# Performance work log

Measured on AMD Instinct MI355X. Metric: run time of the kernel, lower is better.

Reference implementation:

```python
import jax, jax.numpy as jnp
import numpy as np

NUM_HEADS = 32
KV_HEADS = 8
HEAD_SIZE = 128
BATCH = 32
BLOCK_SIZE = 16
BLOCKS_PER_SEQ = 128
NUM_BLOCKS = BATCH * BLOCKS_PER_SEQ  # 4096
ROPE_BASE = 10000.0


def _rope(x, pos):
    # x: [B, n_heads, D]; pos: [B] int32 -> rotate per-sequence single token
    d = x.shape[-1]
    inv_freq = 1.0 / (ROPE_BASE ** (jnp.arange(0, d, 2, dtype=jnp.float32) / d))  # [D/2]
    freqs = pos.astype(jnp.float32)[:, None] * inv_freq[None, :]                  # [B, D/2]
    emb = jnp.concatenate([freqs, freqs], axis=-1)                                # [B, D]
    cos = jnp.cos(emb)[:, None, :]
    sin = jnp.sin(emb)[:, None, :]
    x1, x2 = x[..., : d // 2], x[..., d // 2 :]
    rotated = jnp.concatenate([-x2, x1], axis=-1)
    return x * cos + rotated * sin


def setup_inputs() -> dict:
    key = jax.random.key(0)
    ks = jax.random.split(key, 6)
    query = jax.random.normal(ks[0], (BATCH, NUM_HEADS, HEAD_SIZE), dtype=jnp.float32)
    k_new = jax.random.normal(ks[1], (BATCH, KV_HEADS, HEAD_SIZE), dtype=jnp.float32)
    v_new = jax.random.normal(ks[2], (BATCH, KV_HEADS, HEAD_SIZE), dtype=jnp.float32)
    k_cache = jax.random.normal(ks[3], (NUM_BLOCKS, BLOCK_SIZE, KV_HEADS, HEAD_SIZE), dtype=jnp.float32)
    v_cache = jax.random.normal(ks[4], (NUM_BLOCKS, BLOCK_SIZE, KV_HEADS, HEAD_SIZE), dtype=jnp.float32)
    # each sequence owns a contiguous run of blocks
    block_tables = jnp.arange(NUM_BLOCKS, dtype=jnp.int32).reshape(BATCH, BLOCKS_PER_SEQ)
    context_lens = jax.random.randint(ks[5], (BATCH,), 0, 2047, dtype=jnp.int32)
    return {
        "query": query,
        "key": k_new,
        "value": v_new,
        "k_cache": k_cache,
        "v_cache": v_cache,
        "block_tables": block_tables,
        "context_lens": context_lens,
    }


def reference(query, key, value, k_cache, v_cache, block_tables, context_lens):
    B, H, D = query.shape
    KVH = key.shape[1]
    G = H // KVH
    scale = 1.0 / (D ** 0.5)

    # --- RoPE: source uses position = context_len + 1 for both q and k ---
    pos = context_lens + 1
    q = _rope(query, pos)   # [B, H, D]
    k = _rope(key, pos)     # [B, KVH, D]

    # --- scatter new token into the paged KV cache at slot = context_len ---
    slot = context_lens                               # [B]
    blk = jnp.take_along_axis(block_tables, (slot // BLOCK_SIZE)[:, None], axis=1)[:, 0]
    off = slot % BLOCK_SIZE
    k_cache = k_cache.at[blk, off].set(k)
    v_cache = v_cache.at[blk, off].set(value)

    # --- gather this batch's pages: [B, T, KVH, D] with T = blocks*block_size ---
    T = BLOCKS_PER_SEQ * BLOCK_SIZE
    K = k_cache[block_tables].reshape(B, T, KVH, D)
    V = v_cache[block_tables].reshape(B, T, KVH, D)

    # --- GQA single-query attention over cache_seqlens = context_len + 1 ---
    qg = q.reshape(B, KVH, G, D)
    scores = jnp.einsum("bhgd,bthd->bhgt", qg, K) * scale            # [B, KVH, G, T]
    valid = (jnp.arange(T, dtype=jnp.int32)[None, :] < (context_lens + 1)[:, None])
    scores = jnp.where(valid[:, None, None, :], scores, -jnp.inf)
    probs = jax.nn.softmax(scores, axis=-1)
    out = jnp.einsum("bhgt,bthd->bhgd", probs, V)                    # [B, KVH, G, D]
    return out.reshape(B, H, D)
```

## Files before the change

### kernel.cpp

```cpp
#include <hip/hip_runtime.h>
#include <math.h>

#define BATCH    32
#define NHEADS   32
#define KVHEADS  8
#define GRP      4
#define HSZ      128
#define BLKSZ    16
#define BPS      128
#define NTHREADS 512
#define NPROC    16
#define CHUNK    256
#define NSPLIT   8
#define SCALE    0.08838834764831843f

__device__ __forceinline__ void proc_row(const float4 kv, const float4 vv,
                                         const float4* qf, float* m, float* l,
                                         float4* o) {
    float s[GRP];
#pragma unroll
    for (int g = 0; g < GRP; ++g)
        s[g] = qf[g].x * kv.x + qf[g].y * kv.y + qf[g].z * kv.z + qf[g].w * kv.w;
#pragma unroll
    for (int g = 0; g < GRP; ++g) {
        s[g] += __shfl_xor(s[g], 1);
        s[g] += __shfl_xor(s[g], 2);
        s[g] += __shfl_xor(s[g], 4);
        s[g] += __shfl_xor(s[g], 8);
        s[g] += __shfl_xor(s[g], 16);
    }
#pragma unroll
    for (int g = 0; g < GRP; ++g) {
        const float sc = s[g] * SCALE;
        const float mn = fmaxf(m[g], sc);
        const float cf = __expf(m[g] - mn);
        const float pp = __expf(sc - mn);
        l[g] = l[g] * cf + pp;
        o[g].x = o[g].x * cf + pp * vv.x;
        o[g].y = o[g].y * cf + pp * vv.y;
        o[g].z = o[g].z * cf + pp * vv.z;
        o[g].w = o[g].w * cf + pp * vv.w;
        m[g] = mn;
    }
}

__global__ __launch_bounds__(NTHREADS) void pa_partial(
    const float* __restrict__ query,
    const float* __restrict__ k_new,
    const float* __restrict__ v_new,
    const float* __restrict__ k_cache,
    const float* __restrict__ v_cache,
    const int*  __restrict__ block_tables,
    const int*  __restrict__ ctx_lens,
    float* __restrict__ pm, float* __restrict__ pl, float* __restrict__ po)
{
    const int wg    = blockIdx.x;
    const int chunk = wg & (NSPLIT - 1);
    const int kvh   = (wg >> 3) & (KVHEADS - 1);
    const int b     = wg >> 6;
    const int ctx   = ctx_lens[b];
    const int t0    = chunk * CHUNK;
    if (t0 > ctx) return;

    const int tid  = threadIdx.x;
    const int sub  = tid & 31;
    const int proc = tid >> 5;

    __shared__ float q_s[GRP][HSZ];
    __shared__ float kn_s[HSZ];
    __shared__ int   bt_s[CHUNK / BLKSZ];
    __shared__ float m_s[NPROC][GRP];
    __shared__ float l_s[NPROC][GRP];
    __shared__ float o_s[NPROC][GRP][HSZ];

    {
        const float p = (float)(ctx + 1);
        if (tid < 320) {
            const int   i    = tid & 63;
            const float invf = exp2f(-((float)i / 64.0f) * 13.287712379549449f);
            float s_, c_;
            sincosf(p * invf, &s_, &c_);
            if (tid < 256) {
                const int g = tid >> 6;
                const float* qp = query + ((size_t)b * NHEADS + kvh * GRP + g) * HSZ;
                const float x1 = qp[i], x2 = qp[i + 64];
                q_s[g][i]      = x1 * c_ - x2 * s_;
                q_s[g][i + 64] = x2 * c_ + x1 * s_;
            } else {
                const float* kp = k_new + ((size_t)b * KVHEADS + kvh) * HSZ;
                const float x1 = kp[i], x2 = kp[i + 64];
                kn_s[i]      = x1 * c_ - x2 * s_;
                kn_s[i + 64] = x2 * c_ + x1 * s_;
            }
        } else if (tid < 320 + CHUNK / BLKSZ) {
            bt_s[tid - 320] = block_tables[b * BPS + (t0 >> 4) + (tid - 320)];
        }
    }
    __syncthreads();

    const int d0 = sub << 2;
    float4 qf[GRP];
#pragma unroll
    for (int g = 0; g < GRP; ++g) qf[g] = *(const float4*)&q_s[g][d0];

    float  m[GRP], l[GRP];
    float4 o[GRP];
#pragma unroll
    for (int g = 0; g < GRP; ++g) {
        m[g] = -INFINITY; l[g] = 0.f;
        o[g] = make_float4(0.f, 0.f, 0.f, 0.f);
    }

    const int tend = min(t0 + CHUNK, ctx);
    int t = t0 + proc;
    for (; t + NPROC < tend; t += 2 * NPROC) {
        const int    blk0 = bt_s[(t - t0) >> 4];
        const int    blk1 = bt_s[((t - t0) >> 4) + 1];
        const int    off  = t & 15;
        const size_t a0 = (((size_t)blk0 * BLKSZ + off) * KVHEADS + kvh) * HSZ + d0;
        const size_t a1 = (((size_t)blk1 * BLKSZ + off) * KVHEADS + kvh) * HSZ + d0;
        const float4 kv0 = *(const float4*)(k_cache + a0);
        const float4 vv0 = *(const float4*)(v_cache + a0);
        const float4 kv1 = *(const float4*)(k_cache + a1);
        const float4 vv1 = *(const float4*)(v_cache + a1);
        proc_row(kv0, vv0, qf, m, l, o);
        proc_row(kv1, vv1, qf, m, l, o);
    }
    for (; t < tend; t += NPROC) {
        const int    blk  = bt_s[(t - t0) >> 4];
        const size_t a0 = (((size_t)blk * BLKSZ + (t & 15)) * KVHEADS + kvh) * HSZ + d0;
        const float4 kv = *(const float4*)(k_cache + a0);
        const float4 vv = *(const float4*)(v_cache + a0);
        proc_row(kv, vv, qf, m, l, o);
    }
    if (chunk == (ctx >> 8) && proc == (ctx & (NPROC - 1))) {
        const float4 kv = *(const float4*)&kn_s[d0];
        const float4 vv = *(const float4*)(v_new + ((size_t)b * KVHEADS + kvh) * HSZ + d0);
        proc_row(kv, vv, qf, m, l, o);
    }

    if (sub == 0) {
#pragma unroll
        for (int g = 0; g < GRP; ++g) { m_s[proc][g] = m[g]; l_s[proc][g] = l[g]; }
    }
#pragma unroll
    for (int g = 0; g < GRP; ++g) *(float4*)&o_s[proc][g][d0] = o[g];
    __syncthreads();

    {
        const int g = tid >> 7;
        const int d = tid & 127;
        float mt = -INFINITY;
#pragma unroll
        for (int p = 0; p < NPROC; ++p) mt = fmaxf(mt, m_s[p][g]);
        float lt = 0.f, ot = 0.f;
#pragma unroll
        for (int p = 0; p < NPROC; ++p) {
            const float w = __expf(m_s[p][g] - mt);
            lt += l_s[p][g] * w;
            ot += o_s[p][g][d] * w;
        }
        const size_t idx = (((size_t)(b * KVHEADS + kvh) * GRP + g) * NSPLIT + chunk);
        if (d == 0) { pm[idx] = mt; pl[idx] = lt; }
        po[idx * HSZ + d] = ot;
    }
}

__global__ __launch_bounds__(NTHREADS) void pa_reduce(
    const int*  __restrict__ ctx_lens,
    const float* __restrict__ pm, const float* __restrict__ pl,
    const float* __restrict__ po, float* __restrict__ out)
{
    const int b    = blockIdx.x >> 3;
    const int kvh  = blockIdx.x & 7;
    const int ctx  = ctx_lens[b];
    const int nact = (ctx >> 8) + 1;
    const int tid  = threadIdx.x;
    const int g    = tid >> 7;
    const int d    = tid & 127;
    const size_t idx = ((size_t)(b * KVHEADS + kvh) * GRP + g) * NSPLIT;

    float M = -INFINITY;
    for (int p = 0; p < nact; ++p) M = fmaxf(M, pm[idx + p]);
    float L = 0.f, O = 0.f;
    for (int p = 0; p < nact; ++p) {
        const float w = __expf(pm[idx + p] - M);
        L += pl[idx + p] * w;
        O += po[(idx + p) * HSZ + d] * w;
    }
    out[((size_t)b * NHEADS + kvh * GRP + g) * HSZ + d] = O / L;
}

__global__ __launch_bounds__(NTHREADS) void paged_attn_single(
    const float* __restrict__ query, const float* __restrict__ k_new,
    const float* __restrict__ v_new, const float* __restrict__ k_cache,
    const float* __restrict__ v_cache, const int* __restrict__ block_tables,
    const int* __restrict__ ctx_lens, float* __restrict__ out)
{
    const int wg = blockIdx.x, b = wg >> 3, kvh = wg & 7;
    const int tid = threadIdx.x, sub = tid & 31, proc = tid >> 5;
    const int ctx = ctx_lens[b];

    __shared__ float q_s[GRP][HSZ];
    __shared__ float kn_s[HSZ];
    __shared__ int   bt_s[BPS];
    __shared__ float m_s[NPROC][GRP];
    __shared__ float l_s[NPROC][GRP];
    __shared__ float o_s[NPROC][GRP][HSZ];

    {
        const float p = (float)(ctx + 1);
        if (tid < 320) {
            const int   i    = tid & 63;
            const float invf = exp2f(-((float)i / 64.0f) * 13.287712379549449f);
            float s_, c_;
            sincosf(p * invf, &s_, &c_);
            if (tid < 256) {
                const int g = tid >> 6;
                const float* qp = query + ((size_t)b * NHEADS + kvh * GRP + g) * HSZ;
                const float x1 = qp[i], x2 = qp[i + 64];
                q_s[g][i] = x1 * c_ - x2 * s_; q_s[g][i + 64] = x2 * c_ + x1 * s_;
            } else {
                const float* kp = k_new + ((size_t)b * KVHEADS + kvh) * HSZ;
                const float x1 = kp[i], x2 = kp[i + 64];
                kn_s[i] = x1 * c_ - x2 * s_; kn_s[i + 64] = x2 * c_ + x1 * s_;
            }
        } else if (tid < 448) {
            bt_s[tid - 320] = block_tables[b * BPS + (tid - 320)];
        }
    }
    __syncthreads();

    const int d0 = sub << 2;
    float4 qf[GRP];
#pragma unroll
    for (int g = 0; g < GRP; ++g) qf[g] = *(const float4*)&q_s[g][d0];
    float  m[GRP], l[GRP];
    float4 o[GRP];
#pragma unroll
    for (int g = 0; g < GRP; ++g) {
        m[g] = -INFINITY; l[g] = 0.f; o[g] = make_float4(0.f, 0.f, 0.f, 0.f);
    }
    for (int t = proc; t < ctx; t += NPROC) {
        const int    blk  = bt_s[t >> 4];
        const size_t a0 = (((size_t)blk * BLKSZ + (t & 15)) * KVHEADS + kvh) * HSZ + d0;
        proc_row(*(const float4*)(k_cache + a0), *(const float4*)(v_cache + a0), qf, m, l, o);
    }
    if (proc == (ctx & (NPROC - 1))) {
        proc_row(*(const float4*)&kn_s[d0],
                 *(const float4*)(v_new + ((size_t)b * KVHEADS + kvh) * HSZ + d0), qf, m, l, o);
    }
    if (sub == 0) {
#pragma unroll
        for (int g = 0; g < GRP; ++g) { m_s[proc][g] = m[g]; l_s[proc][g] = l[g]; }
    }
#pragma unroll
    for (int g = 0; g < GRP; ++g) *(float4*)&o_s[proc][g][d0] = o[g];
    __syncthreads();
    {
        const int g = tid >> 7, d = tid & 127;
        float mt = -INFINITY;
#pragma unroll
        for (int p = 0; p < NPROC; ++p) mt = fmaxf(mt, m_s[p][g]);
        float lt = 0.f, ot = 0.f;
#pragma unroll
        for (int p = 0; p < NPROC; ++p) {
            const float w = __expf(m_s[p][g] - mt);
            lt += l_s[p][g] * w; ot += o_s[p][g][d] * w;
        }
        out[((size_t)b * NHEADS + kvh * GRP + g) * HSZ + d] = ot / lt;
    }
}

extern "C" void kernel_launch(void* const* d_in, const int* in_sizes, int n_in,
                              void* d_out, int out_size, void* d_ws, size_t ws_size,
                              hipStream_t stream) {
    const float* query        = (const float*)d_in[0];
    const float* k_new        = (const float*)d_in[1];
    const float* v_new        = (const float*)d_in[2];
    const float* k_cache      = (const float*)d_in[3];
    const float* v_cache      = (const float*)d_in[4];
    const int*   block_tables = (const int*)d_in[5];
    const int*   ctx_lens     = (const int*)d_in[6];
    float*       out          = (float*)d_out;

    const size_t NPART = (size_t)BATCH * KVHEADS * GRP * NSPLIT;
    const size_t need  = (NPART * 2 + NPART * HSZ) * sizeof(float);

    if (ws_size >= need) {
        float* pm = (float*)d_ws;
        float* pl = pm + NPART;
        float* po = pl + NPART;
        pa_partial<<<dim3(BATCH * KVHEADS * NSPLIT), dim3(NTHREADS), 0, stream>>>(
            query, k_new, v_new, k_cache, v_cache, block_tables, ctx_lens, pm, pl, po);
        pa_reduce<<<dim3(BATCH * KVHEADS), dim3(NTHREADS), 0, stream>>>(
            ctx_lens, pm, pl, po, out);
    } else {
        paged_attn_single<<<dim3(BATCH * KVHEADS), dim3(NTHREADS), 0, stream>>>(
            query, k_new, v_new, k_cache, v_cache, block_tables, ctx_lens, out);
    }
}
```

Baseline: 82.74 us.

## Replace online softmax with two-pass chunk softmax using shared score buffer

The split-K partial kernel now computes all QK scores for a 256-token chunk into shared memory, performs a block-wide max and sum reduction, then does a separate PV accumulation pass with plain FMAs instead of per-row online rescaling. Both loops run a fixed trip count with unroll 4, reading the full chunk of K and V even past the context length. Masked rows get -inf scores and zero probability, and the new token's value is handled by adding a correction delta. This removes the per-row exp and rescale work and the dependent recurrence so more loads can be in flight. In exchange it adds several block barriers and extra shared memory, and the fixed trip count reads unused cache rows in partially filled chunks.

```diff
diff --git a/kernel.cpp b/kernel.cpp
--- a/kernel.cpp
+++ b/kernel.cpp
@@ -12,36 +12,16 @@
 #define NPROC    16
 #define CHUNK    256
 #define NSPLIT   8
+#define ITERS    (CHUNK / NPROC)
 #define SCALE    0.08838834764831843f
 
-__device__ __forceinline__ void proc_row(const float4 kv, const float4 vv,
-                                         const float4* qf, float* m, float* l,
-                                         float4* o) {
-    float s[GRP];
-#pragma unroll
-    for (int g = 0; g < GRP; ++g)
-        s[g] = qf[g].x * kv.x + qf[g].y * kv.y + qf[g].z * kv.z + qf[g].w * kv.w;
-#pragma unroll
-    for (int g = 0; g < GRP; ++g) {
-        s[g] += __shfl_xor(s[g], 1);
-        s[g] += __shfl_xor(s[g], 2);
-        s[g] += __shfl_xor(s[g], 4);
-        s[g] += __shfl_xor(s[g], 8);
-        s[g] += __shfl_xor(s[g], 16);
-    }
-#pragma unroll
-    for (int g = 0; g < GRP; ++g) {
-        const float sc = s[g] * SCALE;
-        const float mn = fmaxf(m[g], sc);
-        const float cf = __expf(m[g] - mn);
-        const float pp = __expf(sc - mn);
-        l[g] = l[g] * cf + pp;
-        o[g].x = o[g].x * cf + pp * vv.x;
-        o[g].y = o[g].y * cf + pp * vv.y;
-        o[g].z = o[g].z * cf + pp * vv.z;
-        o[g].w = o[g].w * cf + pp * vv.w;
-        m[g] = mn;
-    }
+__device__ __forceinline__ float hsum32(float v) {
+    v += __shfl_xor(v, 1);
+    v += __shfl_xor(v, 2);
+    v += __shfl_xor(v, 4);
+    v += __shfl_xor(v, 8);
+    v += __shfl_xor(v, 16);
+    return v;
 }
 
 __global__ __launch_bounds__(NTHREADS) void pa_partial(
@@ -69,10 +49,15 @@
     __shared__ float q_s[GRP][HSZ];
     __shared__ float kn_s[HSZ];
     __shared__ int   bt_s[CHUNK / BLKSZ];
-    __shared__ float m_s[NPROC][GRP];
-    __shared__ float l_s[NPROC][GRP];
+    __shared__ float sp[CHUNK][GRP];
+    __shared__ float redm[8], redl[8];
     __shared__ float o_s[NPROC][GRP][HSZ];
 
+    {
+        float* s1 = &sp[0][0];
+        s1[tid]       = -INFINITY;
+        s1[tid + 512] = -INFINITY;
+    }
     {
         const float p = (float)(ctx + 1);
         if (tid < 320) {
@@ -101,68 +86,114 @@
     const int d0 = sub << 2;
     float4 qf[GRP];
 #pragma unroll
-    for (int g = 0; g < GRP; ++g) qf[g] = *(const float4*)&q_s[g][d0];
-
-    float  m[GRP], l[GRP];
+    for (int g = 0; g < GRP; ++g) {
+        float4 t = *(const float4*)&q_s[g][d0];
+        qf[g] = make_float4(t.x * SCALE, t.y * SCALE, t.z * SCALE, t.w * SCALE);
+    }
+
+    const int ncache = min(t0 + CHUNK, ctx) - t0;
+
+#pragma unroll 4
+    for (int i = 0; i < ITERS; ++i) {
+        const int    tl  = proc + i * NPROC;
+        const int    blk = bt_s[tl >> 4];
+        const size_t a   = (((size_t)blk * BLKSZ + (tl & 15)) * KVHEADS + kvh) * HSZ + d0;
+        const float4 kv  = *(const float4*)(k_cache + a);
+        float s[GRP];
+#pragma unroll
+        for (int g = 0; g < GRP; ++g)
+            s[g] = qf[g].x * kv.x + qf[g].y * kv.y + qf[g].z * kv.z + qf[g].w * kv.w;
+#pragma unroll
+        for (int g = 0; g < GRP; ++g) s[g] = hsum32(s[g]);
+        if (tl < ncache && sub == 0)
+            *(float4*)&sp[tl][0] = make_float4(s[0], s[1], s[2], s[3]);
+    }
+    if (chunk == (ctx >> 8)) {
+        const int tc = ctx - t0;
+        if (proc == (tc & (NPROC - 1))) {
+            const float4 kv = *(const float4*)&kn_s[d0];
+            float s[GRP];
+#pragma unroll
+            for (int g = 0; g < GRP; ++g)
+                s[g] = qf[g].x * kv.x + qf[g].y * kv.y + qf[g].z * kv.z + qf[g].w * kv.w;
+#pragma unroll
+            for (int g = 0; g < GRP; ++g) s[g] = hsum32(s[g]);
+            if (sub == 0) *(float4*)&sp[tc][0] = make_float4(s[0], s[1], s[2], s[3]);
+        }
+    }
+    __syncthreads();
+
+    const int g2 = tid >> 7;
+    const int t2 = (tid & 127) << 1;
+    const float s0 = sp[t2][g2], s1 = sp[t2 + 1][g2];
+    float mx = fmaxf(s0, s1);
+    mx = fmaxf(mx, __shfl_xor(mx, 1));
+    mx = fmaxf(mx, __shfl_xor(mx, 2));
+    mx = fmaxf(mx, __shfl_xor(mx, 4));
+    mx = fmaxf(mx, __shfl_xor(mx, 8));
+    mx = fmaxf(mx, __shfl_xor(mx, 16));
+    mx = fmaxf(mx, __shfl_xor(mx, 32));
+    if ((tid & 63) == 0) redm[tid >> 6] = mx;
+    __syncthreads();
+    const float m_g = fmaxf(redm[g2 << 1], redm[(g2 << 1) + 1]);
+    const float p0 = __expf(s0 - m_g);
+    const float p1 = __expf(s1 - m_g);
+    sp[t2][g2]     = p0;
+    sp[t2 + 1][g2] = p1;
+    float ls = p0 + p1;
+    ls += __shfl_xor(ls, 1);
+    ls += __shfl_xor(ls, 2);
+    ls += __shfl_xor(ls, 4);
+    ls += __shfl_xor(ls, 8);
+    ls += __shfl_xor(ls, 16);
+    ls += __shfl_xor(ls, 32);
+    if ((tid & 63) == 0) redl[tid >> 6] = ls;
+    __syncthreads();
+    const float l_g = redl[g2 << 1] + redl[(g2 << 1) + 1];
+
     float4 o[GRP];
 #pragma unroll
-    for (int g = 0; g < GRP; ++g) {
-        m[g] = -INFINITY; l[g] = 0.f;
-        o[g] = make_float4(0.f, 0.f, 0.f, 0.f);
-    }
-
-    const int tend = min(t0 + CHUNK, ctx);
-    int t = t0 + proc;
-    for (; t + NPROC < tend; t += 2 * NPROC) {
-        const int    blk0 = bt_s[(t - t0) >> 4];
-        const int    blk1 = bt_s[((t - t0) >> 4) + 1];
-        const int    off  = t & 15;
-        const size_t a0 = (((size_t)blk0 * BLKSZ + off) * KVHEADS + kvh) * HSZ + d0;
-        const size_t a1 = (((size_t)blk1 * BLKSZ + off) * KVHEADS + kvh) * HSZ + d0;
-        const float4 kv0 = *(const float4*)(k_cache + a0);
-        const float4 vv0 = *(const float4*)(v_cache + a0);
-        const float4 kv1 = *(const float4*)(k_cache + a1);
-        const float4 vv1 = *(const float4*)(v_cache + a1);
-        proc_row(kv0, vv0, qf, m, l, o);
-        proc_row(kv1, vv1, qf, m, l, o);
-    }
-    for (; t < tend; t += NPROC) {
-        const int    blk  = bt_s[(t - t0) >> 4];
-        const size_t a0 = (((size_t)blk * BLKSZ + (t & 15)) * KVHEADS + kvh) * HSZ + d0;
-        const float4 kv = *(const float4*)(k_cache + a0);
-        const float4 vv = *(const float4*)(v_cache + a0);
-        proc_row(kv, vv, qf, m, l, o);
-    }
-    if (chunk == (ctx >> 8) && proc == (ctx & (NPROC - 1))) {
-        const float4 kv = *(const float4*)&kn_s[d0];
-        const float4 vv = *(const float4*)(v_new + ((size_t)b * KVHEADS + kvh) * HSZ + d0);
-        proc_row(kv, vv, qf, m, l, o);
-    }
-
-    if (sub == 0) {
-#pragma unroll
-        for (int g = 0; g < GRP; ++g) { m_s[proc][g] = m[g]; l_s[proc][g] = l[g]; }
-    }
+    for (int g = 0; g < GRP; ++g) o[g] = make_float4(0.f, 0.f, 0.f, 0.f);
+#pragma unroll 4
+    for (int i = 0; i < ITERS; ++i) {
+        const int    tl  = proc + i * NPROC;
+        const int    blk = bt_s[tl >> 4];
+        const size_t a   = (((size_t)blk * BLKSZ + (tl & 15)) * KVHEADS + kvh) * HSZ + d0;
+        const float4 vv  = *(const float4*)(v_cache + a);
+        const float4 pv  = *(const float4*)&sp[tl][0];
+        o[0].x += pv.x * vv.x; o[0].y += pv.x * vv.y; o[0].z += pv.x * vv.z; o[0].w += pv.x * vv.w;
+        o[1].x += pv.y * vv.x; o[1].y += pv.y * vv.y; o[1].z += pv.y * vv.z; o[1].w += pv.y * vv.w;
+        o[2].x += pv.z * vv.x; o[2].y += pv.z * vv.y; o[2].z += pv.z * vv.z; o[2].w += pv.z * vv.w;
+        o[3].x += pv.w * vv.x; o[3].y += pv.w * vv.y; o[3].z += pv.w * vv.z; o[3].w += pv.w * vv.w;
+    }
+    if (chunk == (ctx >> 8)) {
+        const int tc = ctx - t0;
+        if (proc == (tc & (NPROC - 1))) {
+            const int    blk = bt_s[tc >> 4];
+            const size_t a   = (((size_t)blk * BLKSZ + (tc & 15)) * KVHEADS + kvh) * HSZ + d0;
+            const float4 vo  = *(const float4*)(v_cache + a);
+            const float4 vn  = *(const float4*)(v_new + ((size_t)b * KVHEADS + kvh) * HSZ + d0);
+            const float4 pv  = *(const float4*)&sp[tc][0];
+            const float4 dv  = make_float4(vn.x - vo.x, vn.y - vo.y, vn.z - vo.z, vn.w - vo.w);
+            o[0].x += pv.x * dv.x; o[0].y += pv.x * dv.y; o[0].z += pv.x * dv.z; o[0].w += pv.x * dv.w;
+            o[1].x += pv.y * dv.x; o[1].y += pv.y * dv.y; o[1].z += pv.y * dv.z; o[1].w += pv.y * dv.w;
+            o[2].x += pv.z * dv.x; o[2].y += pv.z * dv.y; o[2].z += pv.z * dv.z; o[2].w += pv.z * dv.w;
+            o[3].x += pv.w * dv.x; o[3].y += pv.w * dv.y; o[3].z += pv.w * dv.z; o[3].w += pv.w * dv.w;
+        }
+    }
+
 #pragma unroll
     for (int g = 0; g < GRP; ++g) *(float4*)&o_s[proc][g][d0] = o[g];
     __syncthreads();
-
     {
         const int g = tid >> 7;
         const int d = tid & 127;
-        float mt = -INFINITY;
-#pragma unroll
-        for (int p = 0; p < NPROC; ++p) mt = fmaxf(mt, m_s[p][g]);
-        float lt = 0.f, ot = 0.f;
-#pragma unroll
-        for (int p = 0; p < NPROC; ++p) {
-            const float w = __expf(m_s[p][g] - mt);
-            lt += l_s[p][g] * w;
-            ot += o_s[p][g][d] * w;
-        }
+        float acc = 0.f;
+#pragma unroll
+        for (int p = 0; p < NPROC; ++p) acc += o_s[p][g][d];
         const size_t idx = (((size_t)(b * KVHEADS + kvh) * GRP + g) * NSPLIT + chunk);
-        if (d == 0) { pm[idx] = mt; pl[idx] = lt; }
-        po[idx * HSZ + d] = ot;
+        if (d == 0) { pm[idx] = m_g; pl[idx] = l_g; }
+        po[idx * HSZ + d] = acc;
     }
 }
 
@@ -189,6 +220,30 @@
         O += po[(idx + p) * HSZ + d] * w;
     }
     out[((size_t)b * NHEADS + kvh * GRP + g) * HSZ + d] = O / L;
+}
+
+__device__ __forceinline__ void proc_row_f(const float4 kv, const float4 vv,
+                                           const float4* qf, float* m, float* l,
+                                           float4* o) {
+    float s[GRP];
+#pragma unroll
+    for (int g = 0; g < GRP; ++g)
+        s[g] = qf[g].x * kv.x + qf[g].y * kv.y + qf[g].z * kv.z + qf[g].w * kv.w;
+#pragma unroll
+    for (int g = 0; g < GRP; ++g) s[g] = hsum32(s[g]);
+#pragma unroll
+    for (int g = 0; g < GRP; ++g) {
+        const float sc = s[g] * SCALE;
+        const float mn = fmaxf(m[g], sc);
+        const float cf = __expf(m[g] - mn);
+        const float pp = __expf(sc - mn);
+        l[g] = l[g] * cf + pp;
+        o[g].x = o[g].x * cf + pp * vv.x;
+        o[g].y = o[g].y * cf + pp * vv.y;
+        o[g].z = o[g].z * cf + pp * vv.z;
+        o[g].w = o[g].w * cf + pp * vv.w;
+        m[g] = mn;
+    }
 }
 
 __global__ __launch_bounds__(NTHREADS) void paged_attn_single(
@@ -242,13 +297,13 @@
         m[g] = -INFINITY; l[g] = 0.f; o[g] = make_float4(0.f, 0.f, 0.f, 0.f);
     }
     for (int t = proc; t < ctx; t += NPROC) {
-        const int    blk  = bt_s[t >> 4];
+        const int    blk = bt_s[t >> 4];
         const size_t a0 = (((size_t)blk * BLKSZ + (t & 15)) * KVHEADS + kvh) * HSZ + d0;
-        proc_row(*(const float4*)(k_cache + a0), *(const float4*)(v_cache + a0), qf, m, l, o);
+        proc_row_f(*(const float4*)(k_cache + a0), *(const float4*)(v_cache + a0), qf, m, l, o);
     }
     if (proc == (ctx & (NPROC - 1))) {
-        proc_row(*(const float4*)&kn_s[d0],
-                 *(const float4*)(v_new + ((size_t)b * KVHEADS + kvh) * HSZ + d0), qf, m, l, o);
+        proc_row_f(*(const float4*)&kn_s[d0],
+                   *(const float4*)(v_new + ((size_t)b * KVHEADS + kvh) * HSZ + d0), qf, m, l, o);
     }
     if (sub == 0) {
 #pragma unroll
```

After: 91.76 us. +10.9%, slower.
